# Performance work log

Hardware: AMD Instinct MI355X
Metric: run time of the kernel (lower is better)

Reference implementation:

```python
import jax, jax.numpy as jnp
import numpy as np

B, NQ, NK = 16, 2048, 2048
KD, QD, KQ = 256, 256, 256
CLIP = 10.0


def setup_inputs() -> dict:
    key = jax.random.key(0)
    k1, k2, k3, k4, k5 = jax.random.split(key, 5)
    k_inputs = jax.random.normal(k1, (B, NK, KD), dtype=jnp.float32)
    q_inputs = jax.random.normal(k2, (B, NQ, QD), dtype=jnp.float32)
    adjancy = jax.random.randint(k3, (B, NQ, NK), 0, 2, dtype=jnp.int32)
    # Linear init in source: (rand - 0.5) * 0.05 -> uniform(-0.025, 0.025)
    Wk = jax.random.uniform(k4, (KD, KQ), dtype=jnp.float32, minval=-0.025, maxval=0.025)
    Wq = jax.random.uniform(k5, (QD, KQ), dtype=jnp.float32, minval=-0.025, maxval=0.025)
    return {"k_inputs": k_inputs, "q_inputs": q_inputs, "adjancy": adjancy, "Wk": Wk, "Wq": Wq}


def reference(k_inputs, q_inputs, adjancy, Wk, Wq):
    k = jnp.einsum("bnd,de->bne", k_inputs, Wk)          # [B, NK, KQ]
    q = jnp.einsum("bmd,de->bme", q_inputs, Wq)          # [B, NQ, KQ]
    scale = 1.0 / jnp.sqrt(jnp.asarray(KQ, dtype=q.dtype))
    scores = jnp.einsum("bme,bne->bmn", q, k) * scale     # [B, NQ, NK]
    scores = jnp.tanh(scores) * CLIP                      # clip is not None
    scores = jnp.where(adjancy.astype(bool), scores, -jnp.inf)
    return jax.nn.softmax(scores, axis=2)
```

## Files before the change

### kernel.cpp

```cpp
#include <hip/hip_runtime.h>

#define BATCH 16
#define NQ 2048
#define NK 2048

typedef short s16x8 __attribute__((ext_vector_type(8)));
typedef __bf16 bf16x8 __attribute__((ext_vector_type(8)));
typedef float f32x16 __attribute__((ext_vector_type(16)));
typedef float f32x4 __attribute__((ext_vector_type(4)));
typedef int i32x4 __attribute__((ext_vector_type(4)));
typedef unsigned u32x2 __attribute__((ext_vector_type(2)));

static __device__ __forceinline__ unsigned short f2bf(float f) {
  unsigned u = __builtin_bit_cast(unsigned, f);
  u += 0x7FFFu + ((u >> 16) & 1u);
  return (unsigned short)(u >> 16);
}

static __device__ __forceinline__ f32x16 mfma32(s16x8 a, s16x8 b, f32x16 c) {
  return __builtin_amdgcn_mfma_f32_32x32x16_bf16(
      __builtin_bit_cast(bf16x8, a), __builtin_bit_cast(bf16x8, b), c, 0, 0, 0);
}

static __device__ __forceinline__ f32x4 mfma16(s16x8 a, s16x8 b, f32x4 c) {
  return __builtin_amdgcn_mfma_f32_16x16x32_bf16(
      __builtin_bit_cast(bf16x8, a), __builtin_bit_cast(bf16x8, b), c, 0, 0, 0);
}

static __device__ __forceinline__ float score_p(float s) {
  float u = __builtin_amdgcn_exp2f(s * 2.885390081777927f);
  return __builtin_amdgcn_exp2f(-28.853900817779268f * __builtin_amdgcn_rcpf(u + 1.0f));
}

__global__ void prep_wt(const float* __restrict__ Wk, unsigned short* __restrict__ WkT,
                        const float* __restrict__ Wq, unsigned short* __restrict__ WqT) {
  const float* W = blockIdx.y ? Wq : Wk;
  unsigned short* WT = blockIdx.y ? WqT : WkT;
  float scale = blockIdx.y ? 0.0625f : 1.0f;
  int idx = blockIdx.x * 256 + threadIdx.x;
  int n = idx >> 8, k = idx & 255;
  WT[n * 256 + k] = f2bf(W[k * 256 + n] * scale);
}

__global__ __launch_bounds__(256) void pack_adj(const int* __restrict__ adj,
                                                unsigned* __restrict__ mask) {
  int gwave = (blockIdx.x * 256 + threadIdx.x) >> 6;
  int lane = threadIdx.x & 63;
  const int* p = adj + (size_t)gwave * 2048;
  unsigned my = 0;
#pragma unroll
  for (int c = 0; c < 32; ++c) {
    int a = p[c * 64 + lane];
    unsigned long long m = __ballot(a != 0);
    if ((lane >> 1) == c) my = (lane & 1) ? (unsigned)(m >> 32) : (unsigned)m;
  }
  mask[(size_t)gwave * 64 + lane] = my;
}

__global__ __launch_bounds__(256, 2) void proj_kernel(
    const float* __restrict__ Xk, const unsigned short* __restrict__ WkT,
    unsigned short* __restrict__ Yk,
    const float* __restrict__ Xq, const unsigned short* __restrict__ WqT,
    unsigned short* __restrict__ Yq) {
  const float* X;
  const unsigned short* WT;
  unsigned short* Y;
  if (blockIdx.y == 0) { X = Xk; WT = WkT; Y = Yk; }
  else                 { X = Xq; WT = WqT; Y = Yq; }

  int tid = threadIdx.x;
  int wave = tid >> 6, lane = tid & 63;
  int l31 = lane & 31, kh = lane >> 5;
  int r0 = blockIdx.x * 128 + wave * 32;

  const float* xp = X + (size_t)(r0 + l31) * 256 + kh * 8;

  f32x16 acc[8];
#pragma unroll
  for (int ct = 0; ct < 8; ++ct)
#pragma unroll
    for (int i = 0; i < 16; ++i) acc[ct][i] = 0.0f;

#pragma unroll
  for (int kk = 0; kk < 16; ++kk) {
    f32x4 a0 = *(const f32x4*)(xp + kk * 16);
    f32x4 a1 = *(const f32x4*)(xp + kk * 16 + 4);
    s16x8 af;
#pragma unroll
    for (int j = 0; j < 4; ++j) {
      af[j]     = (short)f2bf(a0[j]);
      af[4 + j] = (short)f2bf(a1[j]);
    }
#pragma unroll
    for (int ct = 0; ct < 8; ++ct) {
      s16x8 bw = *(const s16x8*)(WT + (size_t)(ct * 32 + l31) * 256 + kk * 16 + kh * 8);
      acc[ct] = mfma32(af, bw, acc[ct]);
    }
  }

  int kg2 = l31 >> 3, j = l31 & 7;
#pragma unroll
  for (int ct = 0; ct < 8; ++ct) {
#pragma unroll
    for (int r = 0; r < 16; ++r) {
      int rrow = (r & 3) + 8 * (r >> 2) + 4 * kh;
      int row = r0 + rrow;
      Y[((size_t)((row >> 4) * 8 + ct) * 64 + kg2 * 16 + (row & 15)) * 8 + j] =
          f2bf(acc[ct][r]);
    }
  }
}

__global__ __launch_bounds__(512, 1) void attn_kernel(
    const unsigned short* __restrict__ Kf, const unsigned short* __restrict__ Qf,
    const unsigned* __restrict__ mask, float* __restrict__ out) {
  int lin = blockIdx.y * 64 + blockIdx.x;
  int b  = (lin & 7) * 2 + ((lin >> 3) & 1);
  int qt = lin >> 4;
  int q0 = qt * 32;
  int tid = threadIdx.x;
  int wave = tid >> 6, lane = tid & 63;
  int l15 = lane & 15, kg = lane >> 4;
  int colbase = wave * 256;

  __shared__ unsigned plds[8 * 16 * 256];
  __shared__ unsigned lmask[32 * 68];
  __shared__ float wsum[8][32];
  __shared__ float rrecip[32];

  {
    const i32x4* msrc = (const i32x4*)(mask + ((size_t)b * NQ + q0) * 64);
    i32x4 v = msrc[tid];
    int row = tid >> 4, w4 = tid & 15;
    *(i32x4*)(lmask + row * 68 + w4 * 4) = v;
  }

  const unsigned short* qpA = Qf + (size_t)(b * 128 + 2 * qt) * 4096;
  s16x8 aqA[8], aqB[8];
#pragma unroll
  for (int kk = 0; kk < 8; ++kk) {
    aqA[kk] = __builtin_nontemporal_load(
        (const s16x8*)(qpA + ((size_t)kk * 64 + lane) * 8));
    aqB[kk] = __builtin_nontemporal_load(
        (const s16x8*)(qpA + 4096 + ((size_t)kk * 64 + lane) * 8));
  }

  __syncthreads();

  const unsigned short* kfb = Kf + (size_t)b * 128 * 4096;
  unsigned* pl = plds + wave * 4096 + lane * 2;

  float rsumA[4] = {0.0f, 0.0f, 0.0f, 0.0f};
  float rsumB[4] = {0.0f, 0.0f, 0.0f, 0.0f};
  s16x8 bkX[8], bkY[8];

#define KLOAD(CT, DST)                                                         \
  {                                                                            \
    const unsigned short* kpt = kfb + (size_t)(wave * 16 + (CT)) * 4096;       \
    _Pragma("unroll") for (int kk = 0; kk < 8; ++kk)                           \
        DST[kk] = *(const s16x8*)(kpt + ((size_t)kk * 64 + lane) * 8);         \
  }

#define PROCESS(CT, BK)                                                        \
  {                                                                            \
    f32x4 accA = {0.0f, 0.0f, 0.0f, 0.0f};                                     \
    f32x4 accB = {0.0f, 0.0f, 0.0f, 0.0f};                                     \
    _Pragma("unroll") for (int kk = 0; kk < 8; ++kk) {                         \
      accA = mfma16(aqA[kk], BK[kk], accA);                                    \
      accB = mfma16(aqB[kk], BK[kk], accB);                                    \
    }                                                                          \
    unsigned shift = (unsigned)(((CT) & 1) * 16 + l15);                        \
    int wrd = wave * 8 + ((CT) >> 1);                                          \
    float pA[4], pB[4];                                                        \
    _Pragma("unroll") for (int r = 0; r < 4; ++r) {                            \
      unsigned mwA = lmask[(kg * 4 + r) * 68 + wrd];                           \
      unsigned mwB = lmask[(16 + kg * 4 + r) * 68 + wrd];                      \
      float eA = score_p(accA[r]);                                             \
      float eB = score_p(accB[r]);                                             \
      pA[r] = ((mwA >> shift) & 1u) ? eA : 0.0f;                               \
      pB[r] = ((mwB >> shift) & 1u) ? eB : 0.0f;                               \
      rsumA[r] += pA[r];                                                       \
      rsumB[r] += pB[r];                                                       \
    }                                                                          \
    u32x2 vA, vB;                                                              \
    vA[0] = (unsigned)f2bf(pA[0]) | ((unsigned)f2bf(pA[1]) << 16);             \
    vA[1] = (unsigned)f2bf(pA[2]) | ((unsigned)f2bf(pA[3]) << 16);             \
    vB[0] = (unsigned)f2bf(pB[0]) | ((unsigned)f2bf(pB[1]) << 16);             \
    vB[1] = (unsigned)f2bf(pB[2]) | ((unsigned)f2bf(pB[3]) << 16);             \
    *(u32x2*)(pl + (CT)*256) = vA;                                             \
    *(u32x2*)(pl + (CT)*256 + 128) = vB;                                       \
  }

  KLOAD(0, bkX)
#pragma unroll
  for (int cp = 0; cp < 8; ++cp) {
    KLOAD(2 * cp + 1, bkY)
    PROCESS(2 * cp, bkX)
    if (cp < 7) KLOAD(2 * cp + 2, bkX)
    PROCESS(2 * cp + 1, bkY)
  }
#undef KLOAD
#undef PROCESS

#pragma unroll
  for (int r = 0; r < 4; ++r) {
    float vA = rsumA[r], vB = rsumB[r];
    vA += __shfl_xor(vA, 1);  vB += __shfl_xor(vB, 1);
    vA += __shfl_xor(vA, 2);  vB += __shfl_xor(vB, 2);
    vA += __shfl_xor(vA, 4);  vB += __shfl_xor(vB, 4);
    vA += __shfl_xor(vA, 8);  vB += __shfl_xor(vB, 8);
    rsumA[r] = vA;  rsumB[r] = vB;
  }
  if (l15 == 0) {
#pragma unroll
    for (int r = 0; r < 4; ++r) {
      wsum[wave][kg * 4 + r]      = rsumA[r];
      wsum[wave][16 + kg * 4 + r] = rsumB[r];
    }
  }
  __syncthreads();
  if (tid < 32) {
    float s = 0.0f;
#pragma unroll
    for (int w = 0; w < 8; ++w) s += wsum[w][tid];
    rrecip[tid] = 1.0f / s;
  }
  __syncthreads();

  float rcA[4], rcB[4];
#pragma unroll
  for (int r = 0; r < 4; ++r) {
    rcA[r] = rrecip[kg * 4 + r];
    rcB[r] = rrecip[16 + kg * 4 + r];
  }

  float* opA = out + ((size_t)b * NQ + q0 + kg * 4) * (size_t)NK + colbase + l15;
  float* opB = opA + (size_t)16 * NK;
#pragma unroll 4
  for (int ct = 0; ct < 16; ++ct) {
    u32x2 vA = *(const u32x2*)(pl + ct * 256);
    u32x2 vB = *(const u32x2*)(pl + ct * 256 + 128);
#pragma unroll
    for (int r = 0; r < 4; ++r) {
      unsigned w = (r < 2) ? vA[0] : vA[1];
      float p = __builtin_bit_cast(float, (r & 1) ? (w & 0xffff0000u) : (w << 16));
      opA[(size_t)r * NK + ct * 16] = p * rcA[r];
    }
#pragma unroll
    for (int r = 0; r < 4; ++r) {
      unsigned w = (r < 2) ? vB[0] : vB[1];
      float p = __builtin_bit_cast(float, (r & 1) ? (w & 0xffff0000u) : (w << 16));
      opB[(size_t)r * NK + ct * 16] = p * rcB[r];
    }
  }
}

extern "C" void kernel_launch(void* const* d_in, const int* in_sizes, int n_in,
                              void* d_out, int out_size, void* d_ws, size_t ws_size,
                              hipStream_t stream) {
  const float* k_in = (const float*)d_in[0];
  const float* q_in = (const float*)d_in[1];
  const int* adj    = (const int*)d_in[2];
  const float* Wk   = (const float*)d_in[3];
  const float* Wq   = (const float*)d_in[4];
  float* out = (float*)d_out;

  char* ws = (char*)d_ws;
  unsigned short* WkT = (unsigned short*)(ws);
  unsigned short* WqT = (unsigned short*)(ws + (1u << 17));
  unsigned short* Kf  = (unsigned short*)(ws + (1u << 18));
  unsigned short* Qf  = (unsigned short*)(ws + (1u << 18) + (1u << 24));
  unsigned* maskbuf   = (unsigned*)(ws + (1u << 18) + (2u << 24));

  prep_wt<<<dim3(256, 2), 256, 0, stream>>>(Wk, WkT, Wq, WqT);

  pack_adj<<<(BATCH * NQ * NK) / (2048 * 4), 256, 0, stream>>>(adj, maskbuf);

  proj_kernel<<<dim3(256, 2), 256, 0, stream>>>(k_in, WkT, Kf, q_in, WqT, Qf);

  attn_kernel<<<dim3(64, 16), 512, 0, stream>>>(Kf, Qf, maskbuf, out);
}
```

Baseline: 251.3 us.

## Fuse weight transpose, adjacency packing and projection into one prep kernel

Merges the three preprocessing launches (weight transpose/convert, adjacency bit-packing, projection GEMM) into a single kernel with a block-index split. Each projection block now transposes and converts its weight slice into swizzled LDS in four k-chunks instead of reading a pre-transposed global copy. This removes two kernel launches and the serial dependency between them. The cost is redundant per-block weight conversion, extra syncthreads, and 32KB of LDS per block, which may lower occupancy.

```diff
diff --git a/kernel.cpp b/kernel.cpp
--- a/kernel.cpp
+++ b/kernel.cpp
@@ -32,46 +32,41 @@
   return __builtin_amdgcn_exp2f(-28.853900817779268f * __builtin_amdgcn_rcpf(u + 1.0f));
 }
 
-__global__ void prep_wt(const float* __restrict__ Wk, unsigned short* __restrict__ WkT,
-                        const float* __restrict__ Wq, unsigned short* __restrict__ WqT) {
-  const float* W = blockIdx.y ? Wq : Wk;
-  unsigned short* WT = blockIdx.y ? WqT : WkT;
-  float scale = blockIdx.y ? 0.0625f : 1.0f;
-  int idx = blockIdx.x * 256 + threadIdx.x;
-  int n = idx >> 8, k = idx & 255;
-  WT[n * 256 + k] = f2bf(W[k * 256 + n] * scale);
-}
-
-__global__ __launch_bounds__(256) void pack_adj(const int* __restrict__ adj,
-                                                unsigned* __restrict__ mask) {
-  int gwave = (blockIdx.x * 256 + threadIdx.x) >> 6;
-  int lane = threadIdx.x & 63;
-  const int* p = adj + (size_t)gwave * 2048;
-  unsigned my = 0;
-#pragma unroll
-  for (int c = 0; c < 32; ++c) {
-    int a = p[c * 64 + lane];
-    unsigned long long m = __ballot(a != 0);
-    if ((lane >> 1) == c) my = (lane & 1) ? (unsigned)(m >> 32) : (unsigned)m;
-  }
-  mask[(size_t)gwave * 64 + lane] = my;
-}
-
-__global__ __launch_bounds__(256, 2) void proj_kernel(
-    const float* __restrict__ Xk, const unsigned short* __restrict__ WkT,
-    unsigned short* __restrict__ Yk,
-    const float* __restrict__ Xq, const unsigned short* __restrict__ WqT,
-    unsigned short* __restrict__ Yq) {
+__global__ __launch_bounds__(256, 2) void prep_all(
+    const float* __restrict__ Xk, const float* __restrict__ Xq,
+    const float* __restrict__ Wk, const float* __restrict__ Wq,
+    const int* __restrict__ adj,
+    unsigned short* __restrict__ Yk, unsigned short* __restrict__ Yq,
+    unsigned* __restrict__ mask) {
+  __shared__ unsigned short wtl[256 * 64];
+  int bid = blockIdx.x;
+  int tid = threadIdx.x;
+
+  if (bid >= 512) {
+    int gwave = ((bid - 512) * 256 + tid) >> 6;
+    int lane = tid & 63;
+    const int* p = adj + (size_t)gwave * 2048;
+    unsigned my = 0;
+#pragma unroll
+    for (int c = 0; c < 32; ++c) {
+      int a = p[c * 64 + lane];
+      unsigned long long m = __ballot(a != 0);
+      if ((lane >> 1) == c) my = (lane & 1) ? (unsigned)(m >> 32) : (unsigned)m;
+    }
+    mask[(size_t)gwave * 64 + lane] = my;
+    return;
+  }
+
   const float* X;
-  const unsigned short* WT;
+  const float* W;
   unsigned short* Y;
-  if (blockIdx.y == 0) { X = Xk; WT = WkT; Y = Yk; }
-  else                 { X = Xq; WT = WqT; Y = Yq; }
-
-  int tid = threadIdx.x;
+  float scale;
+  if (bid < 256) { X = Xk; W = Wk; Y = Yk; scale = 1.0f; }
+  else           { X = Xq; W = Wq; Y = Yq; scale = 0.0625f; }
+  int xb = bid & 255;
   int wave = tid >> 6, lane = tid & 63;
   int l31 = lane & 31, kh = lane >> 5;
-  int r0 = blockIdx.x * 128 + wave * 32;
+  int r0 = xb * 128 + wave * 32;
 
   const float* xp = X + (size_t)(r0 + l31) * 256 + kh * 8;
 
@@ -81,20 +76,35 @@
 #pragma unroll
     for (int i = 0; i < 16; ++i) acc[ct][i] = 0.0f;
 
-#pragma unroll
-  for (int kk = 0; kk < 16; ++kk) {
-    f32x4 a0 = *(const f32x4*)(xp + kk * 16);
-    f32x4 a1 = *(const f32x4*)(xp + kk * 16 + 4);
-    s16x8 af;
-#pragma unroll
-    for (int j = 0; j < 4; ++j) {
-      af[j]     = (short)f2bf(a0[j]);
-      af[4 + j] = (short)f2bf(a1[j]);
-    }
-#pragma unroll
-    for (int ct = 0; ct < 8; ++ct) {
-      s16x8 bw = *(const s16x8*)(WT + (size_t)(ct * 32 + l31) * 256 + kk * 16 + kh * 8);
-      acc[ct] = mfma32(af, bw, acc[ct]);
+#pragma unroll 1
+  for (int s = 0; s < 4; ++s) {
+    __syncthreads();
+#pragma unroll 16
+    for (int kl = 0; kl < 64; ++kl) {
+      int k = s * 64 + kl;
+      float w = W[(size_t)k * 256 + tid] * scale;
+      wtl[tid * 64 + (((kl >> 3) ^ (tid & 7)) << 3) + (kl & 7)] = f2bf(w);
+    }
+    __syncthreads();
+
+#pragma unroll
+    for (int kq = 0; kq < 4; ++kq) {
+      int kk = s * 4 + kq;
+      f32x4 a0 = *(const f32x4*)(xp + kk * 16);
+      f32x4 a1 = *(const f32x4*)(xp + kk * 16 + 4);
+      s16x8 af;
+#pragma unroll
+      for (int j = 0; j < 4; ++j) {
+        af[j]     = (short)f2bf(a0[j]);
+        af[4 + j] = (short)f2bf(a1[j]);
+      }
+      int bk = kq * 2 + kh;
+#pragma unroll
+      for (int ct = 0; ct < 8; ++ct) {
+        int n = ct * 32 + l31;
+        s16x8 bw = *(const s16x8*)(wtl + n * 64 + ((bk ^ (n & 7)) << 3));
+        acc[ct] = mfma32(af, bw, acc[ct]);
+      }
     }
   }
 
@@ -266,17 +276,12 @@
   float* out = (float*)d_out;
 
   char* ws = (char*)d_ws;
-  unsigned short* WkT = (unsigned short*)(ws);
-  unsigned short* WqT = (unsigned short*)(ws + (1u << 17));
   unsigned short* Kf  = (unsigned short*)(ws + (1u << 18));
   unsigned short* Qf  = (unsigned short*)(ws + (1u << 18) + (1u << 24));
   unsigned* maskbuf   = (unsigned*)(ws + (1u << 18) + (2u << 24));
 
-  prep_wt<<<dim3(256, 2), 256, 0, stream>>>(Wk, WkT, Wq, WqT);
-
-  pack_adj<<<(BATCH * NQ * NK) / (2048 * 4), 256, 0, stream>>>(adj, maskbuf);
-
-  proj_kernel<<<dim3(256, 2), 256, 0, stream>>>(k_in, WkT, Kf, q_in, WqT, Qf);
+  prep_all<<<512 + 8192, 256, 0, stream>>>(k_in, q_in, Wk, Wq, adj,
+                                           Kf, Qf, maskbuf);
 
   attn_kernel<<<dim3(64, 16), 512, 0, stream>>>(Kf, Qf, maskbuf, out);
 }
```

Result: faster. 220.6 us (-12.2%).
